# Optimization experiments

Hardware: AMD Instinct MI355X
Metric: run time of the kernel (lower is better)

Reference implementation:

```python
import jax, jax.numpy as jnp
import numpy as np

EPS = 1e-10
PAD = -1.0


def setup_inputs() -> dict:
    key = jax.random.key(0)
    k1, k2, k3 = jax.random.split(key, 3)
    M, N = 512, 8192
    outputs = jax.random.normal(k1, (M, N), dtype=jnp.float32)
    config_runtime = jax.random.uniform(k2, (M, N), dtype=jnp.float32)
    config_idxs = jax.random.randint(k3, (M, N), 0, 4096, dtype=jnp.int64)
    return {"outputs": outputs, "config_runtime": config_runtime, "config_idxs": config_idxs}


def _dedup_mask(config_idxs):
    # True at every occurrence of a config id except the first (by index order),
    # per row. Equivalent to the torch per-row unique/nonzero loop, vectorized
    # via a stable sort + adjacent-equal + inverse-permutation scatter.
    order = jnp.argsort(config_idxs, axis=1)            # stable sort by value
    sorted_idx = jnp.take_along_axis(config_idxs, order, axis=1)
    dup_sorted = jnp.concatenate(
        [jnp.zeros((config_idxs.shape[0], 1), dtype=bool),
         sorted_idx[:, 1:] == sorted_idx[:, :-1]], axis=1)
    inv = jnp.argsort(order, axis=1)                    # inverse permutation
    return jnp.take_along_axis(dup_sorted, inv, axis=1)


def reference(outputs, config_runtime, config_idxs):
    M, N = outputs.shape
    # 1) mark duplicate config ids as padded in y_true
    y_true = jnp.where(_dedup_mask(config_idxs), PAD, config_runtime)
    # 2) random column shuffle (torch.randperm analogue; fixed key for determinism)
    perm = jax.random.permutation(jax.random.key(42), N)
    y_pred_s = outputs[:, perm]
    y_true_s = y_true[:, perm]
    # 3) sort descending by y_true, gather preds into that order
    idx = jnp.argsort(-y_true_s, axis=1)
    y_true_sorted = jnp.take_along_axis(y_true_s, idx, axis=1)
    mask = y_true_sorted == PAD
    preds = jnp.take_along_axis(y_pred_s, idx, axis=1)
    preds = jnp.where(mask, -jnp.inf, preds)
    # 4) stable reverse-cumsum log-sum-exp
    mx = jnp.max(preds, axis=1, keepdims=True)
    pmm = jnp.where(mask, 0.0, preds - mx)              # safe: masked -> 0
    exps = jnp.where(mask, 0.0, jnp.exp(pmm))
    cums = jnp.flip(jnp.cumsum(jnp.flip(exps, axis=1), axis=1), axis=1)
    obs = jnp.where(mask, 0.0, jnp.log(cums + EPS) - pmm)
    return jnp.mean(jnp.sum(obs, axis=1))
```

## Files before the change

### kernel.cpp

```cpp
#include <hip/hip_runtime.h>

#define MROWS 512
#define NCOLS 8192
#define NVALS 4096
#define BLOCK 512
#define NW 8
#define EPSF 1e-10f

typedef unsigned int u32;
typedef unsigned long long u64;

__device__ __forceinline__ int TP(int e) { return ((e & 7) << 9) | (e >> 3); }

__global__ __launch_bounds__(BLOCK, 4) void listmle_row_kernel(
    const float* __restrict__ outputs,
    const float* __restrict__ runtime,
    const int*   __restrict__ idxs,
    float* __restrict__ row_out)
{
    __shared__ u32 A[NVALS];
    __shared__ u32 C[NVALS + 8];
    __shared__ u64 KA[NVALS];
    __shared__ float s_max[NW], s_ps[NW], s_fs[NW], s_lg[NW];
    __shared__ u32 s_cnt[NW];

    const int tid = threadIdx.x, lane = tid & 63, wave = tid >> 6;
    const int row = blockIdx.x;
    const float* rp = outputs + (size_t)row * NCOLS;
    const float* rr = runtime + (size_t)row * NCOLS;
    const int*   ri = idxs    + (size_t)row * NCOLS;

    int vidx[16]; float vrt[16], vpred[16];
    #pragma unroll
    for (int q = 0; q < 4; ++q) {
        const int b0 = (q << 11) + (tid << 2);
        int4   i4 = *reinterpret_cast<const int4*>(ri + b0);
        float4 r4 = *reinterpret_cast<const float4*>(rr + b0);
        float4 p4 = *reinterpret_cast<const float4*>(rp + b0);
        vidx[q*4+0]=i4.x;  vidx[q*4+1]=i4.y;  vidx[q*4+2]=i4.z;  vidx[q*4+3]=i4.w;
        vrt [q*4+0]=r4.x;  vrt [q*4+1]=r4.y;  vrt [q*4+2]=r4.z;  vrt [q*4+3]=r4.w;
        vpred[q*4+0]=p4.x; vpred[q*4+1]=p4.y; vpred[q*4+2]=p4.z; vpred[q*4+3]=p4.w;
    }
    #pragma unroll
    for (int i = 0; i < 8; ++i) { A[(i<<9)+tid] = 0xFFFFFFFFu; C[(i<<9)+tid] = 0u; }
    if (tid < 8) C[NVALS + tid] = 0u;
    __syncthreads();

    #pragma unroll
    for (int m = 0; m < 16; ++m) {
        const u32 j = ((m >> 2) << 11) + (tid << 2) + (m & 3);
        atomicMin(&A[vidx[m]], j);
    }
    __syncthreads();

    u32 vkey[16];
    float lmax = -INFINITY, psum = 0.f;
    u32 kept = 0;
    #pragma unroll
    for (int m = 0; m < 16; ++m) {
        lmax = fmaxf(lmax, vpred[m]);
        u32 rt24 = (u32)(vrt[m] * 16777216.0f);
        rt24 = rt24 > 0xFFFFFFu ? 0xFFFFFFu : rt24;
        vkey[m] = rt24;
        const u32 j = ((m >> 2) << 11) + (tid << 2) + (m & 3);
        if (A[vidx[m]] == j) {
            kept |= 1u << m;
            psum += vpred[m];
            atomicAdd(&C[TP((int)(rt24 >> 12))], 1u);
        }
    }
    #pragma unroll
    for (int off = 32; off > 0; off >>= 1) {
        lmax = fmaxf(lmax, __shfl_down(lmax, off));
        psum += __shfl_down(psum, off);
    }
    if (lane == 0) { s_max[wave] = lmax; s_ps[wave] = psum; }
    __syncthreads();

    float mx = s_max[0];
    #pragma unroll
    for (int w = 1; w < NW; ++w) mx = fmaxf(mx, s_max[w]);

    u32 c8[8], lsum = 0;
    #pragma unroll
    for (int i = 0; i < 8; ++i) { c8[i] = C[(i<<9)+tid]; lsum += c8[i]; }
    #pragma unroll
    for (int i = 0; i < 8; ++i) A[(i<<9)+tid] = 0u;
    u32 xs = lsum;
    #pragma unroll
    for (int off = 1; off < 64; off <<= 1) { u32 y = __shfl_up(xs, off); if (lane >= off) xs += y; }
    if (lane == 63) s_cnt[wave] = xs;
    __syncthreads();

    u32 run = xs - lsum, K = 0;
    #pragma unroll
    for (int w = 0; w < NW; ++w) { const u32 t = s_cnt[w]; if (w < wave) run += t; K += t; }
    #pragma unroll
    for (int i = 0; i < 8; ++i) { const u32 c = c8[i]; C[(i<<9)+tid] = run; run += c; }
    if (tid == 0) C[NVALS] = K;
    __syncthreads();

    #pragma unroll
    for (int m = 0; m < 16; ++m) {
        if (kept & (1u << m)) {
            const u32 j = ((m >> 2) << 11) + (tid << 2) + (m & 3);
            const u32 rt24 = vkey[m];
            const int b = (int)(rt24 >> 12);
            const u32 base = C[TP(b)];
            const u32 ra = atomicAdd(&A[TP(b)], 1u);
            const u32 ck = ((rt24 & 0xFFFu) << 13) | j;
            const float e = __expf(vpred[m] - mx);
            KA[base + ra] = ((u64)ck << 32) | (u64)__float_as_uint(e);
        }
    }
    __syncthreads();

    float pf[16];
    #pragma unroll
    for (int m = 0; m < 16; ++m) {
        if (kept & (1u << m)) {
            const u32 j = ((m >> 2) << 11) + (tid << 2) + (m & 3);
            const u32 rt24 = vkey[m];
            const int b = (int)(rt24 >> 12);
            const u32 base = C[TP(b)];
            const u32 lim  = (b == NVALS - 1) ? C[NVALS] : C[TP(b + 1)];
            const u32 ck = ((rt24 & 0xFFFu) << 13) | j;
            double dsm = 0.0;
            u32 r = 0;
            for (u32 q = base; q < lim; ++q) {
                const u64 v = KA[q];
                if ((u32)(v >> 32) < ck) { dsm += (double)__uint_as_float((u32)v); ++r; }
            }
            const float pfm = (float)(dsm + (double)__expf(vpred[m] - mx));
            pf[m] = pfm;
            if (r == lim - base - 1)
                A[TP(b)] = __float_as_uint(pfm);
        }
    }
    __syncthreads();

    float f8[8], fsum = 0.f;
    #pragma unroll
    for (int i = 0; i < 8; ++i) { f8[i] = __uint_as_float(A[(i<<9)+tid]); fsum += f8[i]; }
    float xf = fsum;
    #pragma unroll
    for (int off = 1; off < 64; off <<= 1) { float y = __shfl_up(xf, off); if (lane >= off) xf += y; }
    if (lane == 63) s_fs[wave] = xf;
    __syncthreads();

    float frun = xf - fsum;
    #pragma unroll
    for (int w = 0; w < NW; ++w) if (w < wave) frun += s_fs[w];
    #pragma unroll
    for (int i = 0; i < 8; ++i) { const float c = f8[i]; A[(i<<9)+tid] = __float_as_uint(frun); frun += c; }
    __syncthreads();

    float logacc = 0.f;
    #pragma unroll
    for (int m = 0; m < 16; ++m) {
        if (kept & (1u << m)) {
            const float S = __uint_as_float(A[TP((int)(vkey[m] >> 12))]);
            logacc += __logf(S + pf[m] + EPSF);
        }
    }
    #pragma unroll
    for (int off = 32; off > 0; off >>= 1) logacc += __shfl_down(logacc, off);
    if (lane == 0) s_lg[wave] = logacc;
    __syncthreads();

    if (tid == 0) {
        float lt = 0.f, pt = 0.f;
        #pragma unroll
        for (int w = 0; w < NW; ++w) { lt += s_lg[w]; pt += s_ps[w]; }
        row_out[row] = lt - pt + (float)K * mx;
    }
}

__global__ __launch_bounds__(256) void listmle_finalize(
    const float* __restrict__ row_out, float* __restrict__ out)
{
    __shared__ double red_d[4];
    const int tid = threadIdx.x;
    const int lane = tid & 63, wave = tid >> 6;
    double acc = 0.0;
    for (int r = tid; r < MROWS; r += 256) acc += (double)row_out[r];
    #pragma unroll
    for (int off = 32; off > 0; off >>= 1) acc += __shfl_down(acc, off);
    if (lane == 0) red_d[wave] = acc;
    __syncthreads();
    if (tid == 0) {
        double tot = 0.0;
        for (int w = 0; w < 4; ++w) tot += red_d[w];
        out[0] = (float)(tot / (double)MROWS);
    }
}

extern "C" void kernel_launch(void* const* d_in, const int* in_sizes, int n_in,
                              void* d_out, int out_size, void* d_ws, size_t ws_size,
                              hipStream_t stream) {
    const float* outputs = (const float*)d_in[0];
    const float* runtime = (const float*)d_in[1];
    const int*   idxs    = (const int*)d_in[2];
    float* out = (float*)d_out;
    float* ws  = (float*)d_ws;

    listmle_row_kernel<<<MROWS, BLOCK, 0, stream>>>(outputs, runtime, idxs, ws);
    listmle_finalize<<<1, 256, 0, stream>>>(ws, out);
}
```

Before: 31.33 us.

## Shrink LDS footprint with fp16 exp/prefix storage and packed index registers

Replaces the 64-bit key+exp shared array with separate 32-bit key and fp16 exp arrays, reuses buffers for bucket offsets, stores bucket prefix sums in fp16, and packs column ids into 16-bit halves of registers. The launch bound is raised from 4 to 6 blocks per CU to exploit the smaller LDS and register footprint. The self exp is now read back from LDS rather than recomputed. Storing exps and prefix sums in fp16 loses precision in the log-sum-exp terms and risks tolerance failures.

```diff
diff --git a/kernel.cpp b/kernel.cpp
--- a/kernel.cpp
+++ b/kernel.cpp
@@ -1,4 +1,5 @@
 #include <hip/hip_runtime.h>
+#include <hip/hip_fp16.h>
 
 #define MROWS 512
 #define NCOLS 8192
@@ -8,19 +9,22 @@
 #define EPSF 1e-10f
 
 typedef unsigned int u32;
-typedef unsigned long long u64;
+typedef unsigned short u16;
 
 __device__ __forceinline__ int TP(int e) { return ((e & 7) << 9) | (e >> 3); }
-
-__global__ __launch_bounds__(BLOCK, 4) void listmle_row_kernel(
+__device__ __forceinline__ u16 f2h(float x) { return __half_as_ushort(__float2half_rn(x)); }
+__device__ __forceinline__ float h2f(u16 h) { return __half2float(__ushort_as_half(h)); }
+
+__global__ __launch_bounds__(BLOCK, 6) void listmle_row_kernel(
     const float* __restrict__ outputs,
     const float* __restrict__ runtime,
     const int*   __restrict__ idxs,
     float* __restrict__ row_out)
 {
     __shared__ u32 A[NVALS];
-    __shared__ u32 C[NVALS + 8];
-    __shared__ u64 KA[NVALS];
+    __shared__ u32 KEY[NVALS];
+    __shared__ u16 EXPH[NVALS];
+    __shared__ u16 T[NVALS];
     __shared__ float s_max[NW], s_ps[NW], s_fs[NW], s_lg[NW];
     __shared__ u32 s_cnt[NW];
 
@@ -30,43 +34,51 @@
     const float* rr = runtime + (size_t)row * NCOLS;
     const int*   ri = idxs    + (size_t)row * NCOLS;
 
-    int vidx[16]; float vrt[16], vpred[16];
+    u32 pidx[8]; u32 vkey[16]; float vpred[16];
     #pragma unroll
     for (int q = 0; q < 4; ++q) {
         const int b0 = (q << 11) + (tid << 2);
-        int4   i4 = *reinterpret_cast<const int4*>(ri + b0);
-        float4 r4 = *reinterpret_cast<const float4*>(rr + b0);
-        float4 p4 = *reinterpret_cast<const float4*>(rp + b0);
-        vidx[q*4+0]=i4.x;  vidx[q*4+1]=i4.y;  vidx[q*4+2]=i4.z;  vidx[q*4+3]=i4.w;
-        vrt [q*4+0]=r4.x;  vrt [q*4+1]=r4.y;  vrt [q*4+2]=r4.z;  vrt [q*4+3]=r4.w;
+        const int4   i4 = *reinterpret_cast<const int4*>(ri + b0);
+        const float4 r4 = *reinterpret_cast<const float4*>(rr + b0);
+        const float4 p4 = *reinterpret_cast<const float4*>(rp + b0);
+        pidx[q*2]   = ((u32)i4.x & 0xFFFFu) | ((u32)i4.y << 16);
+        pidx[q*2+1] = ((u32)i4.z & 0xFFFFu) | ((u32)i4.w << 16);
+        const float rv[4] = { r4.x, r4.y, r4.z, r4.w };
+        #pragma unroll
+        for (int r = 0; r < 4; ++r) {
+            u32 u = (u32)(rv[r] * 16777216.0f);
+            vkey[q*4+r] = u > 0xFFFFFFu ? 0xFFFFFFu : u;
+        }
         vpred[q*4+0]=p4.x; vpred[q*4+1]=p4.y; vpred[q*4+2]=p4.z; vpred[q*4+3]=p4.w;
     }
     #pragma unroll
-    for (int i = 0; i < 8; ++i) { A[(i<<9)+tid] = 0xFFFFFFFFu; C[(i<<9)+tid] = 0u; }
-    if (tid < 8) C[NVALS + tid] = 0u;
-    __syncthreads();
-
-    #pragma unroll
-    for (int m = 0; m < 16; ++m) {
+    for (int i = 0; i < 8; ++i) { A[(i<<9)+tid] = 0xFFFFFFFFu; KEY[(i<<9)+tid] = 0u; }
+    {
+        u32* t32 = reinterpret_cast<u32*>(T);
+        #pragma unroll
+        for (int i = 0; i < 4; ++i) t32[(i<<9)+tid] = 0u;
+    }
+    __syncthreads();
+
+    #pragma unroll
+    for (int m = 0; m < 16; ++m) {
+        const u32 v = (pidx[m>>1] >> ((m & 1) << 4)) & 0xFFFFu;
         const u32 j = ((m >> 2) << 11) + (tid << 2) + (m & 3);
-        atomicMin(&A[vidx[m]], j);
-    }
-    __syncthreads();
-
-    u32 vkey[16];
+        atomicMin(&A[v], j);
+    }
+    __syncthreads();
+
     float lmax = -INFINITY, psum = 0.f;
     u32 kept = 0;
     #pragma unroll
     for (int m = 0; m < 16; ++m) {
         lmax = fmaxf(lmax, vpred[m]);
-        u32 rt24 = (u32)(vrt[m] * 16777216.0f);
-        rt24 = rt24 > 0xFFFFFFu ? 0xFFFFFFu : rt24;
-        vkey[m] = rt24;
+        const u32 v = (pidx[m>>1] >> ((m & 1) << 4)) & 0xFFFFu;
         const u32 j = ((m >> 2) << 11) + (tid << 2) + (m & 3);
-        if (A[vidx[m]] == j) {
+        if (A[v] == j) {
             kept |= 1u << m;
             psum += vpred[m];
-            atomicAdd(&C[TP((int)(rt24 >> 12))], 1u);
+            atomicAdd(&KEY[TP((int)(vkey[m] >> 12))], 1u);
         }
     }
     #pragma unroll
@@ -83,9 +95,7 @@
 
     u32 c8[8], lsum = 0;
     #pragma unroll
-    for (int i = 0; i < 8; ++i) { c8[i] = C[(i<<9)+tid]; lsum += c8[i]; }
-    #pragma unroll
-    for (int i = 0; i < 8; ++i) A[(i<<9)+tid] = 0u;
+    for (int i = 0; i < 8; ++i) { c8[i] = KEY[(i<<9)+tid]; lsum += c8[i]; }
     u32 xs = lsum;
     #pragma unroll
     for (int off = 1; off < 64; off <<= 1) { u32 y = __shfl_up(xs, off); if (lane >= off) xs += y; }
@@ -96,21 +106,17 @@
     #pragma unroll
     for (int w = 0; w < NW; ++w) { const u32 t = s_cnt[w]; if (w < wave) run += t; K += t; }
     #pragma unroll
-    for (int i = 0; i < 8; ++i) { const u32 c = c8[i]; C[(i<<9)+tid] = run; run += c; }
-    if (tid == 0) C[NVALS] = K;
+    for (int i = 0; i < 8; ++i) { const u32 c = c8[i]; A[(i<<9)+tid] = run; run += c; }
     __syncthreads();
 
     #pragma unroll
     for (int m = 0; m < 16; ++m) {
         if (kept & (1u << m)) {
             const u32 j = ((m >> 2) << 11) + (tid << 2) + (m & 3);
-            const u32 rt24 = vkey[m];
-            const int b = (int)(rt24 >> 12);
-            const u32 base = C[TP(b)];
-            const u32 ra = atomicAdd(&A[TP(b)], 1u);
-            const u32 ck = ((rt24 & 0xFFFu) << 13) | j;
-            const float e = __expf(vpred[m] - mx);
-            KA[base + ra] = ((u64)ck << 32) | (u64)__float_as_uint(e);
+            const u32 k = vkey[m];
+            const u32 pos = atomicAdd(&A[TP((int)(k >> 12))], 1u);
+            KEY[pos]  = ((k & 0xFFFu) << 13) | j;
+            EXPH[pos] = f2h(__expf(vpred[m] - mx));
         }
     }
     __syncthreads();
@@ -120,28 +126,30 @@
     for (int m = 0; m < 16; ++m) {
         if (kept & (1u << m)) {
             const u32 j = ((m >> 2) << 11) + (tid << 2) + (m & 3);
-            const u32 rt24 = vkey[m];
-            const int b = (int)(rt24 >> 12);
-            const u32 base = C[TP(b)];
-            const u32 lim  = (b == NVALS - 1) ? C[NVALS] : C[TP(b + 1)];
-            const u32 ck = ((rt24 & 0xFFFu) << 13) | j;
+            const u32 k = vkey[m];
+            const int b = (int)(k >> 12);
+            const u32 start = b ? A[TP(b - 1)] : 0u;
+            const u32 end   = A[TP(b)];
+            const u32 ck = ((k & 0xFFFu) << 13) | j;
             double dsm = 0.0;
+            float eo = 0.f;
             u32 r = 0;
-            for (u32 q = base; q < lim; ++q) {
-                const u64 v = KA[q];
-                if ((u32)(v >> 32) < ck) { dsm += (double)__uint_as_float((u32)v); ++r; }
+            for (u32 q = start; q < end; ++q) {
+                const u32 k2 = KEY[q];
+                if (k2 < ck) { dsm += (double)h2f(EXPH[q]); ++r; }
+                else if (k2 == ck) eo = h2f(EXPH[q]);
             }
-            const float pfm = (float)(dsm + (double)__expf(vpred[m] - mx));
+            const float pfm = (float)(dsm + (double)eo);
             pf[m] = pfm;
-            if (r == lim - base - 1)
-                A[TP(b)] = __float_as_uint(pfm);
+            if (r == end - start - 1u)
+                T[TP(b)] = f2h(pfm);
         }
     }
     __syncthreads();
 
     float f8[8], fsum = 0.f;
     #pragma unroll
-    for (int i = 0; i < 8; ++i) { f8[i] = __uint_as_float(A[(i<<9)+tid]); fsum += f8[i]; }
+    for (int i = 0; i < 8; ++i) { f8[i] = h2f(T[(i<<9)+tid]); fsum += f8[i]; }
     float xf = fsum;
     #pragma unroll
     for (int off = 1; off < 64; off <<= 1) { float y = __shfl_up(xf, off); if (lane >= off) xf += y; }
@@ -152,14 +160,14 @@
     #pragma unroll
     for (int w = 0; w < NW; ++w) if (w < wave) frun += s_fs[w];
     #pragma unroll
-    for (int i = 0; i < 8; ++i) { const float c = f8[i]; A[(i<<9)+tid] = __float_as_uint(frun); frun += c; }
+    for (int i = 0; i < 8; ++i) { const float c = f8[i]; T[(i<<9)+tid] = f2h(frun); frun += c; }
     __syncthreads();
 
     float logacc = 0.f;
     #pragma unroll
     for (int m = 0; m < 16; ++m) {
         if (kept & (1u << m)) {
-            const float S = __uint_as_float(A[TP((int)(vkey[m] >> 12))]);
+            const float S = h2f(T[TP((int)(vkey[m] >> 12))]);
             logacc += __logf(S + pf[m] + EPSF);
         }
     }
```

Result: slower. 44.54 us (+42.2%).
